# Optimization experiments

Measured on AMD Instinct MI355X. Metric: run time of the kernel, lower is better.

## Reference

```python
import jax, jax.numpy as jnp
import numpy as np


def setup_inputs() -> dict:
    key = jax.random.key(0)
    k1, k2 = jax.random.split(key)
    N = 8192
    preds = jax.random.normal(k1, (N,), dtype=jnp.float32)
    targets = jax.random.normal(k2, (N,), dtype=jnp.float32)
    return {"preds": preds, "targets": targets}


def reference(preds, targets):
    n = preds.shape[0]
    # torch.std is unbiased (ddof=1)
    margin = 0.25 * jnp.std(targets, ddof=1)
    # broadcasted all-pairs differences: [N, N]
    tdiff = targets[:, None] - targets[None, :]
    pdiff = preds[:, None] - preds[None, :]
    loss = jnp.maximum(-jnp.sign(tdiff) * pdiff + margin, 0.0)
    # only pairs with i < j (strict upper triangle)
    mask = jnp.triu(jnp.ones((n, n), dtype=bool), k=1)
    num_pairs = n * (n - 1) // 2
    total = jnp.sum(jnp.where(mask, loss, 0.0))
    return total / num_pairs
```

## Files before the change

kernel.cpp:

```cpp
#include <hip/hip_runtime.h>

#define NT 256
#define SPLIT 2

__device__ __forceinline__ float pair_loss(float tt, float pp, float tj, float pj, float margin) {
    float td = tt - tj;
    float pd = pp - pj;
    float cs = copysignf(1.0f, td);
    return fmaxf(fmaf(-cs, pd, margin), 0.0f);
}

__device__ __forceinline__ void do_j(float tj, float pj, const float* tg, const float* pg,
                                     float margin, float* av) {
    #pragma unroll
    for (int k = 0; k < 8; ++k) av[k] += pair_loss(tg[k], pg[k], tj, pj, margin);
}

__global__ __launch_bounds__(NT, 4)
void pair_kernel(const float* __restrict__ preds, const float* __restrict__ targets,
                 double* __restrict__ partials, int N)
{
    const int tid = threadIdx.x, lane = tid & 63, wave = tid >> 6;
    __shared__ double red[2 * (NT / 64)];
    __shared__ float smargin;

    double s = 0.0, s2 = 0.0;
    const int n4 = N >> 2;
    const float4* t4 = (const float4*)targets;
    for (int i = tid; i < n4; i += NT) {
        float4 v = t4[i];
        s  += (double)v.x + (double)v.y + (double)v.z + (double)v.w;
        s2 += (double)v.x * v.x + (double)v.y * v.y + (double)v.z * v.z + (double)v.w * v.w;
    }
    for (int i = (n4 << 2) + tid; i < N; i += NT) { float t = targets[i]; s += t; s2 += (double)t * t; }
    #pragma unroll
    for (int off = 32; off; off >>= 1) { s += __shfl_down(s, off, 64); s2 += __shfl_down(s2, off, 64); }
    if (lane == 0) { red[wave] = s; red[NT / 64 + wave] = s2; }
    __syncthreads();
    if (tid == 0) {
        double S = 0.0, S2 = 0.0;
        for (int w = 0; w < NT / 64; ++w) { S += red[w]; S2 += red[NT / 64 + w]; }
        double mean = S / (double)N;
        double var  = (S2 - (double)N * mean * mean) / (double)(N - 1);
        smargin = (float)(0.25 * sqrt(var > 0.0 ? var : 0.0));
    }
    __syncthreads();
    const float margin = smargin;

    const int G = N >> 3;
    const int P = G >> 1;
    const int NB = (int)gridDim.x;
    const int sub = (int)(blockIdx.x & (SPLIT - 1));
    const int pairblk = (int)(blockIdx.x >> 1);
    const int PSTRIDE = NB >> 1;

    float av[8];
    #pragma unroll
    for (int k = 0; k < 8; ++k) av[k] = 0.0f;
    double extra = 0.0;

    for (int p = pairblk; p < P; p += PSTRIDE) {
        #pragma unroll
        for (int side = 0; side < 2; ++side) {
            const int gg = side ? (G - 1 - p) : p;
            const int i0 = gg << 3;
            float tg[8], pg[8];
            #pragma unroll
            for (int k = 0; k < 8; ++k) { tg[k] = targets[i0 + k]; pg[k] = preds[i0 + k]; }

            if (sub == side && tid < 64) {
                int ii = tid >> 3, jj = tid & 7;
                if (ii < jj) {
                    float td = tg[ii] - tg[jj], pd = pg[ii] - pg[jj];
                    float cs = (td > 0.0f) ? 1.0f : ((td < 0.0f) ? -1.0f : 0.0f);
                    extra += (double)fmaxf(fmaf(-cs, pd, margin), 0.0f);
                }
            }

            const int lo = i0 + 8;
            const int len = N - lo;
            const int len4 = len >> 2;
            const float4* tj4 = (const float4*)(targets + lo);
            const float4* pj4 = (const float4*)(preds + lo);
            for (int idx = sub * NT + tid; idx < len4; idx += NT * SPLIT) {
                float4 tv = tj4[idx];
                float4 pv = pj4[idx];
                do_j(tv.x, pv.x, tg, pg, margin, av);
                do_j(tv.y, pv.y, tg, pg, margin, av);
                do_j(tv.z, pv.z, tg, pg, margin, av);
                do_j(tv.w, pv.w, tg, pg, margin, av);
            }
            for (int j = lo + (len4 << 2) + sub * NT + tid; j < N; j += NT * SPLIT) {
                do_j(targets[j], preds[j], tg, pg, margin, av);
            }
        }
    }

    if (pairblk == 0) {
        if (G & 1) {
            const int i0 = (G >> 1) << 3;
            for (int k = 0; k < 8 && i0 + k < N; ++k) {
                const int i = i0 + k;
                for (int j = i + 1 + sub * NT + tid; j < N; j += NT * SPLIT) {
                    float td = targets[i] - targets[j], pd = preds[i] - preds[j];
                    float cs = (td > 0.0f) ? 1.0f : ((td < 0.0f) ? -1.0f : 0.0f);
                    extra += (double)fmaxf(fmaf(-cs, pd, margin), 0.0f);
                }
            }
        }
        for (int i = G << 3; i < N; ++i) {
            for (int j = i + 1 + sub * NT + tid; j < N; j += NT * SPLIT) {
                float td = targets[i] - targets[j], pd = preds[i] - preds[j];
                float cs = (td > 0.0f) ? 1.0f : ((td < 0.0f) ? -1.0f : 0.0f);
                extra += (double)fmaxf(fmaf(-cs, pd, margin), 0.0f);
            }
        }
    }

    double tot = extra;
    #pragma unroll
    for (int k = 0; k < 8; ++k) tot += (double)av[k];
    #pragma unroll
    for (int off = 32; off; off >>= 1) tot += __shfl_down(tot, off, 64);
    __syncthreads();
    if (lane == 0) red[wave] = tot;
    __syncthreads();
    if (tid == 0) {
        double bt = 0.0;
        for (int w = 0; w < NT / 64; ++w) bt += red[w];
        partials[blockIdx.x] = bt;
    }
}

__global__ __launch_bounds__(NT)
void finalize_kernel(const double* __restrict__ partials, int nparts,
                     float* __restrict__ out, double inv_pairs)
{
    __shared__ double red[NT / 64];
    const int tid = threadIdx.x, lane = tid & 63, wave = tid >> 6;
    double s = 0.0;
    for (int i = tid; i < nparts; i += NT) s += partials[i];
    #pragma unroll
    for (int off = 32; off; off >>= 1) s += __shfl_down(s, off, 64);
    if (lane == 0) red[wave] = s;
    __syncthreads();
    if (tid == 0) {
        double t = 0.0;
        for (int w = 0; w < NT / 64; ++w) t += red[w];
        out[0] = (float)(t * inv_pairs);
    }
}

extern "C" void kernel_launch(void* const* d_in, const int* in_sizes, int n_in,
                              void* d_out, int out_size, void* d_ws, size_t ws_size,
                              hipStream_t stream) {
    const float* preds   = (const float*)d_in[0];
    const float* targets = (const float*)d_in[1];
    float* out = (float*)d_out;
    int N = in_sizes[0];

    double* partials = (double*)d_ws;
    const int G = N >> 3;
    const int P = G >> 1;

    int NB = (P > 0 ? P : 1) * SPLIT;
    if (NB > 1024) NB = 1024;
    int maxParts = (int)(ws_size / sizeof(double));
    if (NB > maxParts) NB = (maxParts / SPLIT) * SPLIT;
    if (NB < SPLIT) NB = SPLIT;

    const double inv_pairs = 2.0 / ((double)N * (double)(N - 1));
    pair_kernel<<<NB, NT, 0, stream>>>(preds, targets, partials, N);
    finalize_kernel<<<1, NT, 0, stream>>>(partials, NB, out, inv_pairs);
}
```

Baseline: 18.11 us.

## Split pair rows across four blocks, prefetch next float4, use float stats

Each pair of row-groups is now split across four blocks instead of two, and the grid cap is raised to 2048 with launch bounds asking for 8 blocks per CU, so more waves are resident. The inner j loop software-prefetches the next float4 of targets and preds while it computes the current one, to hide load latency. The mean/variance pass and the small 'extra' accumulators now use float instead of double, which cuts slow FP64 work but slightly lowers accuracy. More blocks also means more redundant per-block reduction of the margin statistics.

```diff
diff --git a/kernel.cpp b/kernel.cpp
--- a/kernel.cpp
+++ b/kernel.cpp
@@ -1,7 +1,7 @@
 #include <hip/hip_runtime.h>
 
 #define NT 256
-#define SPLIT 2
+#define SPLIT 4
 
 __device__ __forceinline__ float pair_loss(float tt, float pp, float tj, float pj, float margin) {
     float td = tt - tj;
@@ -16,48 +16,51 @@
     for (int k = 0; k < 8; ++k) av[k] += pair_loss(tg[k], pg[k], tj, pj, margin);
 }
 
-__global__ __launch_bounds__(NT, 4)
+__global__ __launch_bounds__(NT, 8)
 void pair_kernel(const float* __restrict__ preds, const float* __restrict__ targets,
                  double* __restrict__ partials, int N)
 {
     const int tid = threadIdx.x, lane = tid & 63, wave = tid >> 6;
-    __shared__ double red[2 * (NT / 64)];
+    __shared__ double redd[2 * (NT / 64)];
     __shared__ float smargin;
 
-    double s = 0.0, s2 = 0.0;
-    const int n4 = N >> 2;
-    const float4* t4 = (const float4*)targets;
-    for (int i = tid; i < n4; i += NT) {
-        float4 v = t4[i];
-        s  += (double)v.x + (double)v.y + (double)v.z + (double)v.w;
-        s2 += (double)v.x * v.x + (double)v.y * v.y + (double)v.z * v.z + (double)v.w * v.w;
+    {
+        float s = 0.0f, s2 = 0.0f;
+        const int n4 = N >> 2;
+        const float4* t4 = (const float4*)targets;
+        for (int i = tid; i < n4; i += NT) {
+            float4 v = t4[i];
+            s  += v.x + v.y + v.z + v.w;
+            s2 += v.x * v.x + v.y * v.y + v.z * v.z + v.w * v.w;
+        }
+        for (int i = (n4 << 2) + tid; i < N; i += NT) { float t = targets[i]; s += t; s2 += t * t; }
+        double ds = (double)s, ds2 = (double)s2;
+        #pragma unroll
+        for (int off = 32; off; off >>= 1) { ds += __shfl_down(ds, off, 64); ds2 += __shfl_down(ds2, off, 64); }
+        if (lane == 0) { redd[wave] = ds; redd[NT / 64 + wave] = ds2; }
+        __syncthreads();
+        if (tid == 0) {
+            double S = 0.0, S2 = 0.0;
+            for (int w = 0; w < NT / 64; ++w) { S += redd[w]; S2 += redd[NT / 64 + w]; }
+            double mean = S / (double)N;
+            double var  = (S2 - (double)N * mean * mean) / (double)(N - 1);
+            smargin = (float)(0.25 * sqrt(var > 0.0 ? var : 0.0));
+        }
+        __syncthreads();
     }
-    for (int i = (n4 << 2) + tid; i < N; i += NT) { float t = targets[i]; s += t; s2 += (double)t * t; }
-    #pragma unroll
-    for (int off = 32; off; off >>= 1) { s += __shfl_down(s, off, 64); s2 += __shfl_down(s2, off, 64); }
-    if (lane == 0) { red[wave] = s; red[NT / 64 + wave] = s2; }
-    __syncthreads();
-    if (tid == 0) {
-        double S = 0.0, S2 = 0.0;
-        for (int w = 0; w < NT / 64; ++w) { S += red[w]; S2 += red[NT / 64 + w]; }
-        double mean = S / (double)N;
-        double var  = (S2 - (double)N * mean * mean) / (double)(N - 1);
-        smargin = (float)(0.25 * sqrt(var > 0.0 ? var : 0.0));
-    }
-    __syncthreads();
     const float margin = smargin;
 
     const int G = N >> 3;
     const int P = G >> 1;
     const int NB = (int)gridDim.x;
     const int sub = (int)(blockIdx.x & (SPLIT - 1));
-    const int pairblk = (int)(blockIdx.x >> 1);
-    const int PSTRIDE = NB >> 1;
+    const int pairblk = (int)(blockIdx.x >> 2);
+    const int PSTRIDE = NB >> 2;
 
     float av[8];
     #pragma unroll
     for (int k = 0; k < 8; ++k) av[k] = 0.0f;
-    double extra = 0.0;
+    float extra = 0.0f;
 
     for (int p = pairblk; p < P; p += PSTRIDE) {
         #pragma unroll
@@ -73,7 +76,7 @@
                 if (ii < jj) {
                     float td = tg[ii] - tg[jj], pd = pg[ii] - pg[jj];
                     float cs = (td > 0.0f) ? 1.0f : ((td < 0.0f) ? -1.0f : 0.0f);
-                    extra += (double)fmaxf(fmaf(-cs, pd, margin), 0.0f);
+                    extra += fmaxf(fmaf(-cs, pd, margin), 0.0f);
                 }
             }
 
@@ -82,13 +85,23 @@
             const int len4 = len >> 2;
             const float4* tj4 = (const float4*)(targets + lo);
             const float4* pj4 = (const float4*)(preds + lo);
-            for (int idx = sub * NT + tid; idx < len4; idx += NT * SPLIT) {
+
+            int idx = sub * NT + tid;
+            if (idx < len4) {
                 float4 tv = tj4[idx];
                 float4 pv = pj4[idx];
-                do_j(tv.x, pv.x, tg, pg, margin, av);
-                do_j(tv.y, pv.y, tg, pg, margin, av);
-                do_j(tv.z, pv.z, tg, pg, margin, av);
-                do_j(tv.w, pv.w, tg, pg, margin, av);
+                for (;;) {
+                    const int nidx = idx + NT * SPLIT;
+                    const bool more = nidx < len4;
+                    float4 tn, pn;
+                    if (more) { tn = tj4[nidx]; pn = pj4[nidx]; }
+                    do_j(tv.x, pv.x, tg, pg, margin, av);
+                    do_j(tv.y, pv.y, tg, pg, margin, av);
+                    do_j(tv.z, pv.z, tg, pg, margin, av);
+                    do_j(tv.w, pv.w, tg, pg, margin, av);
+                    if (!more) break;
+                    tv = tn; pv = pn; idx = nidx;
+                }
             }
             for (int j = lo + (len4 << 2) + sub * NT + tid; j < N; j += NT * SPLIT) {
                 do_j(targets[j], preds[j], tg, pg, margin, av);
@@ -104,7 +117,7 @@
                 for (int j = i + 1 + sub * NT + tid; j < N; j += NT * SPLIT) {
                     float td = targets[i] - targets[j], pd = preds[i] - preds[j];
                     float cs = (td > 0.0f) ? 1.0f : ((td < 0.0f) ? -1.0f : 0.0f);
-                    extra += (double)fmaxf(fmaf(-cs, pd, margin), 0.0f);
+                    extra += fmaxf(fmaf(-cs, pd, margin), 0.0f);
                 }
             }
         }
@@ -112,22 +125,22 @@
             for (int j = i + 1 + sub * NT + tid; j < N; j += NT * SPLIT) {
                 float td = targets[i] - targets[j], pd = preds[i] - preds[j];
                 float cs = (td > 0.0f) ? 1.0f : ((td < 0.0f) ? -1.0f : 0.0f);
-                extra += (double)fmaxf(fmaf(-cs, pd, margin), 0.0f);
+                extra += fmaxf(fmaf(-cs, pd, margin), 0.0f);
             }
         }
     }
 
-    double tot = extra;
+    double tot = (double)extra;
     #pragma unroll
     for (int k = 0; k < 8; ++k) tot += (double)av[k];
     #pragma unroll
     for (int off = 32; off; off >>= 1) tot += __shfl_down(tot, off, 64);
     __syncthreads();
-    if (lane == 0) red[wave] = tot;
+    if (lane == 0) redd[wave] = tot;
     __syncthreads();
     if (tid == 0) {
         double bt = 0.0;
-        for (int w = 0; w < NT / 64; ++w) bt += red[w];
+        for (int w = 0; w < NT / 64; ++w) bt += redd[w];
         partials[blockIdx.x] = bt;
     }
 }
@@ -164,7 +177,7 @@
     const int P = G >> 1;
 
     int NB = (P > 0 ? P : 1) * SPLIT;
-    if (NB > 1024) NB = 1024;
+    if (NB > 2048) NB = 2048;
     int maxParts = (int)(ws_size / sizeof(double));
     if (NB > maxParts) NB = (maxParts / SPLIT) * SPLIT;
     if (NB < SPLIT) NB = SPLIT;
```

Result: slower. 25.47 us (+40.6%).
